# Kernel tuning notes

Hardware: AMD Instinct MI355X
Metric: run time of the kernel (lower is better)

The kernel has to match this reference:

```python
import jax, jax.numpy as jnp
import numpy as np

H = 256  # hidden_dim
NH = 4   # num_heads
HD = H // NH  # head dim


def setup_inputs() -> dict:
    key = jax.random.key(0)
    ks = jax.random.split(key, 12)
    B, TD, ID = 65536, 512, 512
    s_t = 1.0 / np.sqrt(TD)
    s_h = 1.0 / np.sqrt(H)
    s_f = 1.0 / np.sqrt(2 * H)
    return {
        "text_features": jax.random.normal(ks[0], (B, TD), jnp.float32),
        "image_features": jax.random.normal(ks[1], (B, ID), jnp.float32),
        "W_text": jax.random.uniform(ks[2], (H, TD), jnp.float32, -s_t, s_t),
        "b_text": jax.random.uniform(ks[3], (H,), jnp.float32, -s_t, s_t),
        "W_img": jax.random.uniform(ks[4], (H, ID), jnp.float32, -s_t, s_t),
        "b_img": jax.random.uniform(ks[5], (H,), jnp.float32, -s_t, s_t),
        "in_proj_w": jax.random.normal(ks[6], (3 * H, H), jnp.float32) * s_h,  # xavier-ish
        "in_proj_b": jnp.zeros((3 * H,), jnp.float32),
        "out_proj_w": jax.random.uniform(ks[7], (H, H), jnp.float32, -s_h, s_h),
        "out_proj_b": jnp.zeros((H,), jnp.float32),
        "W_fuse": jax.random.uniform(ks[8], (H, 2 * H), jnp.float32, -s_f, s_f),
        "b_fuse": jax.random.uniform(ks[9], (H,), jnp.float32, -s_f, s_f),
    }


def _mha_seq1(q_in, kv_in, in_proj_w, in_proj_b, out_proj_w, out_proj_b):
    """nn.MultiheadAttention with query seq_len=1 and kv seq_len=1 (eval mode).
    q_in, kv_in: [B, H]. Softmax over the single key is identically 1."""
    Wq, Wk, Wv = jnp.split(in_proj_w, 3, axis=0)
    bq, bk, bv = jnp.split(in_proj_b, 3, axis=0)
    q = (q_in @ Wq.T + bq).reshape(-1, NH, HD)   # [B, nh, hd]
    k = (kv_in @ Wk.T + bk).reshape(-1, NH, HD)
    v = (kv_in @ Wv.T + bv).reshape(-1, NH, HD)
    scores = jnp.einsum("bnd,bnd->bn", q, k) / np.sqrt(HD)  # [B, nh], one key
    attn = jax.nn.softmax(scores[..., None], axis=-1)       # == 1 exactly
    out = (attn * v).reshape(-1, H)                          # concat heads
    return out @ out_proj_w.T + out_proj_b


def reference(text_features, image_features, W_text, b_text, W_img, b_img,
              in_proj_w, in_proj_b, out_proj_w, out_proj_b, W_fuse, b_fuse):
    tp = text_features @ W_text.T + b_text      # [B, H]
    ip = image_features @ W_img.T + b_img       # [B, H]
    text_att = _mha_seq1(tp, ip, in_proj_w, in_proj_b, out_proj_w, out_proj_b)
    img_att = _mha_seq1(ip, tp, in_proj_w, in_proj_b, out_proj_w, out_proj_b)
    fused = jnp.concatenate([text_att, img_att], axis=1)  # [B, 2H]
    return jax.nn.relu(fused @ W_fuse.T + b_fuse)          # dropout = eval no-op
```

## Files before the change

kernel.cpp:

```cpp
#include <hip/hip_runtime.h>
#include <hip/hip_bf16.h>

typedef __attribute__((ext_vector_type(4))) float floatx4;
typedef __attribute__((ext_vector_type(8))) __bf16 bf16x8;

__device__ __forceinline__ unsigned short f2bf(float x) {
    union { float f; unsigned u; } v; v.f = x;
    unsigned r = v.u + 0x7fffu + ((v.u >> 16) & 1u);
    return (unsigned short)(r >> 16);
}

__global__ void p1_M_c(const float* __restrict__ out_proj_w,
                       const float* __restrict__ out_proj_b,
                       const float* __restrict__ in_proj_w,
                       const float* __restrict__ in_proj_b,
                       float* __restrict__ Mmat, float* __restrict__ cvec) {
    __shared__ float row[256];
    __shared__ float red[256];
    const int i = blockIdx.x, j = threadIdx.x;
    row[j] = out_proj_w[i * 256 + j];
    __syncthreads();
    const float* Wv = in_proj_w + 512 * 256;
    float acc = 0.f;
    #pragma unroll 8
    for (int k = 0; k < 256; ++k) acc = fmaf(row[k], Wv[k * 256 + j], acc);
    Mmat[i * 256 + j] = acc;
    red[j] = row[j] * in_proj_b[512 + j];
    __syncthreads();
    for (int s = 128; s > 0; s >>= 1) {
        if (j < s) red[j] += red[j + s];
        __syncthreads();
    }
    if (j == 0) cvec[i] = red[0] + out_proj_b[i];
}

__global__ void p2_G(const float* __restrict__ W_fuse, const float* __restrict__ Mmat,
                     float* __restrict__ G) {
    __shared__ float row[256];
    const int b = blockIdx.x, j = threadIdx.x;
    const int half = b >> 8, i = b & 255;
    row[j] = W_fuse[i * 512 + half * 256 + j];
    __syncthreads();
    float acc = 0.f;
    #pragma unroll 8
    for (int k = 0; k < 256; ++k) acc = fmaf(row[k], Mmat[k * 256 + j], acc);
    G[half * 65536 + i * 256 + j] = acc;
}

__global__ void p3_A(const float* __restrict__ G,
                     const float* __restrict__ W_img, const float* __restrict__ W_text,
                     const float* __restrict__ W_fuse,
                     const float* __restrict__ b_img, const float* __restrict__ b_text,
                     const float* __restrict__ b_fuse, const float* __restrict__ cvec,
                     unsigned short* __restrict__ Wt, float* __restrict__ b_total) {
    __shared__ float grow[4][256];
    __shared__ float red[256];
    const int b = blockIdx.x, j = threadIdx.x;
    const int half = b & 1;
    const int n0 = (b >> 1) * 4;
    const float* Gh = G + half * 65536;
    #pragma unroll
    for (int rr = 0; rr < 4; ++rr) grow[rr][j] = Gh[(n0 + rr) * 256 + j];
    __syncthreads();
    const float* Wsrc = half ? W_text : W_img;
    float acc0[4] = {0.f, 0.f, 0.f, 0.f}, acc1[4] = {0.f, 0.f, 0.f, 0.f};
    #pragma unroll 4
    for (int m = 0; m < 256; ++m) {
        float w0 = Wsrc[m * 512 + j];
        float w1 = Wsrc[m * 512 + 256 + j];
        #pragma unroll
        for (int rr = 0; rr < 4; ++rr) {
            float g = grow[rr][m];
            acc0[rr] = fmaf(g, w0, acc0[rr]);
            acc1[rr] = fmaf(g, w1, acc1[rr]);
        }
    }
    #pragma unroll
    for (int rr = 0; rr < 4; ++rr) {
        const int n = n0 + rr;
        const int nt = n >> 4, nl = n & 15;
        {
            const int kg = half * 512 + j;
            const int kq = kg >> 5, q = (kg >> 3) & 3, jj = kg & 7;
            Wt[((nt * 32 + kq) * 64 + q * 16 + nl) * 8 + jj] = f2bf(acc0[rr]);
        }
        {
            const int kg = half * 512 + 256 + j;
            const int kq = kg >> 5, q = (kg >> 3) & 3, jj = kg & 7;
            Wt[((nt * 32 + kq) * 64 + q * 16 + nl) * 8 + jj] = f2bf(acc1[rr]);
        }
    }
    if (half == 0) {
        const float* Gi = G;
        const float* Gt = G + 65536;
        for (int rr = 0; rr < 4; ++rr) {
            const int n = n0 + rr;
            red[j] = Gi[n * 256 + j] * b_img[j] + Gt[n * 256 + j] * b_text[j]
                   + (W_fuse[n * 512 + j] + W_fuse[n * 512 + 256 + j]) * cvec[j];
            __syncthreads();
            for (int s = 128; s > 0; s >>= 1) {
                if (j < s) red[j] += red[j + s];
                __syncthreads();
            }
            if (j == 0) b_total[n] = b_fuse[n] + red[0];
            __syncthreads();
        }
    }
}

__global__ __launch_bounds__(256, 2)
void fused_gemm(const float* __restrict__ Ximg, const float* __restrict__ Xtxt,
                const unsigned short* __restrict__ Wt,
                const float* __restrict__ b_total, float* __restrict__ out) {
    __shared__ unsigned short At[2][128 * 64];
    const int bid = blockIdx.x;
    const int rowtile = bid >> 1;
    const int cb = bid & 1;
    const int rowbase = rowtile * 128;
    const int t = threadIdx.x;
    const int lane = t & 63;
    const int wave = t >> 6;
    const int wr = wave >> 1, wc = wave & 1;
    const int ml = lane & 15, q = lane >> 4;
    const int xr = ml & 7;
    const int sr = t >> 4;
    const int sc4 = t & 15;
    const int ntbase = cb * 8 + wc * 4;

    floatx4 ld[8];
    floatx4 acc[4][4];
    #pragma unroll
    for (int a = 0; a < 4; ++a)
        #pragma unroll
        for (int bq = 0; bq < 4; ++bq) acc[a][bq] = (floatx4){0.f, 0.f, 0.f, 0.f};

    auto load_step = [&](int s) {
        const int kb = (s & 7) * 64;
        const float* X = (s < 8) ? Ximg : Xtxt;
        const float* src = X + (size_t)(rowbase + sr) * 512 + kb + sc4 * 4;
        #pragma unroll
        for (int i = 0; i < 8; ++i)
            ld[i] = *(const floatx4*)(src + (size_t)i * 16 * 512);
    };
    auto store_tile = [&](unsigned short* buf) {
        const int c = sc4 >> 1;
        const int hofs = (sc4 & 1) * 4;
        #pragma unroll
        for (int i = 0; i < 8; ++i) {
            const int r = sr + 16 * i;
            const int chunk = c ^ (r & 7);
            float2 p0; p0.x = ld[i].x; p0.y = ld[i].y;
            float2 p1; p1.x = ld[i].z; p1.y = ld[i].w;
            __hip_bfloat162 v0 = __float22bfloat162_rn(p0);
            __hip_bfloat162 v1 = __float22bfloat162_rn(p1);
            __hip_bfloat162* dst = (__hip_bfloat162*)(buf + r * 64 + chunk * 8 + hofs);
            dst[0] = v0;
            dst[1] = v1;
        }
    };
    auto compute_step = [&](const unsigned short* buf, int s) {
        #pragma unroll
        for (int koi = 0; koi < 2; ++koi) {
            bf16x8 af[4];
            #pragma unroll
            for (int mi = 0; mi < 4; ++mi) {
                const int r = wr * 64 + mi * 16 + ml;
                const int chunk = ((koi << 2) | q) ^ xr;
                af[mi] = *(const bf16x8*)(buf + r * 64 + chunk * 8);
            }
            const int kq = 2 * s + koi;
            bf16x8 bfr[4];
            #pragma unroll
            for (int ni = 0; ni < 4; ++ni)
                bfr[ni] = *(const bf16x8*)(Wt + (size_t)((ntbase + ni) * 32 + kq) * 512 + lane * 8);
            #pragma unroll
            for (int mi = 0; mi < 4; ++mi)
                #pragma unroll
                for (int ni = 0; ni < 4; ++ni)
                    acc[mi][ni] = __builtin_amdgcn_mfma_f32_16x16x32_bf16(af[mi], bfr[ni], acc[mi][ni], 0, 0, 0);
        }
    };

    load_step(0);
    store_tile(At[0]);
    for (int s = 0; s < 16; ++s) {
        __syncthreads();
        if (s < 15) load_step(s + 1);
        compute_step(At[s & 1], s);
        if (s < 15) store_tile(At[(s + 1) & 1]);
    }

    const int colbase = cb * 128 + wc * 64;
    #pragma unroll
    for (int ni = 0; ni < 4; ++ni) {
        const int col = colbase + ni * 16 + ml;
        const float bias = b_total[col];
        #pragma unroll
        for (int mi = 0; mi < 4; ++mi) {
            const size_t r0 = (size_t)rowbase + wr * 64 + mi * 16 + q * 4;
            #pragma unroll
            for (int e = 0; e < 4; ++e) {
                float v = acc[mi][ni][e] + bias;
                out[(r0 + e) * 256 + col] = fmaxf(v, 0.f);
            }
        }
    }
}

extern "C" void kernel_launch(void* const* d_in, const int* in_sizes, int n_in,
                              void* d_out, int out_size, void* d_ws, size_t ws_size,
                              hipStream_t stream) {
    const float* text       = (const float*)d_in[0];
    const float* image      = (const float*)d_in[1];
    const float* W_text     = (const float*)d_in[2];
    const float* b_text     = (const float*)d_in[3];
    const float* W_img      = (const float*)d_in[4];
    const float* b_img      = (const float*)d_in[5];
    const float* in_proj_w  = (const float*)d_in[6];
    const float* in_proj_b  = (const float*)d_in[7];
    const float* out_proj_w = (const float*)d_in[8];
    const float* out_proj_b = (const float*)d_in[9];
    const float* W_fuse     = (const float*)d_in[10];
    const float* b_fuse     = (const float*)d_in[11];
    float* out = (float*)d_out;

    float* ws      = (float*)d_ws;
    float* Mmat    = ws;
    float* G       = ws + 65536;
    float* cvec    = ws + 3 * 65536;
    float* b_total = cvec + 256;
    unsigned short* Wt = (unsigned short*)(b_total + 256);

    p1_M_c<<<dim3(256), dim3(256), 0, stream>>>(out_proj_w, out_proj_b, in_proj_w, in_proj_b, Mmat, cvec);
    p2_G<<<dim3(512), dim3(256), 0, stream>>>(W_fuse, Mmat, G);
    p3_A<<<dim3(128), dim3(256), 0, stream>>>(G, W_img, W_text, W_fuse, b_img, b_text, b_fuse, cvec, Wt, b_total);
    fused_gemm<<<dim3(1024), dim3(256), 0, stream>>>(image, text, Wt, b_total, out);
}
```

Before: 404.6 us.

## Reassociate weight folding into tiled GEMMs and make main GEMM LDS-free

The weight-folding precompute is re-associated and split differently. One kernel forms W_fuse·out_proj and Wv·W_img/W_text as shared-memory-tiled SGEMMs, plus the bias vectors. A second tiled kernel multiplies those products into the packed bf16 weight and the total bias. This replaces three poorly parallel row-per-block kernels with two launches. The main MFMA GEMM drops the LDS staging and swizzle: each wave loads its 32 activation rows straight from global into registers, converts them to bf16, and covers 128 output columns with double-buffered register prefetch. The trade-off is less data sharing between waves, more register pressure and possibly less coalesced global reads.

```diff
diff --git a/kernel.cpp b/kernel.cpp
--- a/kernel.cpp
+++ b/kernel.cpp
@@ -2,7 +2,9 @@
 #include <hip/hip_bf16.h>
 
 typedef __attribute__((ext_vector_type(4))) float floatx4;
+typedef __attribute__((ext_vector_type(2))) float floatx2;
 typedef __attribute__((ext_vector_type(8))) __bf16 bf16x8;
+typedef __attribute__((ext_vector_type(8))) unsigned short ushortx8;
 
 __device__ __forceinline__ unsigned short f2bf(float x) {
     union { float f; unsigned u; } v; v.f = x;
@@ -10,194 +12,219 @@
     return (unsigned short)(r >> 16);
 }
 
-__global__ void p1_M_c(const float* __restrict__ out_proj_w,
-                       const float* __restrict__ out_proj_b,
-                       const float* __restrict__ in_proj_w,
-                       const float* __restrict__ in_proj_b,
-                       float* __restrict__ Mmat, float* __restrict__ cvec) {
-    __shared__ float row[256];
-    __shared__ float red[256];
-    const int i = blockIdx.x, j = threadIdx.x;
-    row[j] = out_proj_w[i * 256 + j];
-    __syncthreads();
-    const float* Wv = in_proj_w + 512 * 256;
-    float acc = 0.f;
-    #pragma unroll 8
-    for (int k = 0; k < 256; ++k) acc = fmaf(row[k], Wv[k * 256 + j], acc);
-    Mmat[i * 256 + j] = acc;
-    red[j] = row[j] * in_proj_b[512 + j];
-    __syncthreads();
-    for (int s = 128; s > 0; s >>= 1) {
-        if (j < s) red[j] += red[j + s];
-        __syncthreads();
-    }
-    if (j == 0) cvec[i] = red[0] + out_proj_b[i];
-}
-
-__global__ void p2_G(const float* __restrict__ W_fuse, const float* __restrict__ Mmat,
-                     float* __restrict__ G) {
-    __shared__ float row[256];
-    const int b = blockIdx.x, j = threadIdx.x;
-    const int half = b >> 8, i = b & 255;
-    row[j] = W_fuse[i * 512 + half * 256 + j];
-    __syncthreads();
-    float acc = 0.f;
-    #pragma unroll 8
-    for (int k = 0; k < 256; ++k) acc = fmaf(row[k], Mmat[k * 256 + j], acc);
-    G[half * 65536 + i * 256 + j] = acc;
-}
-
-__global__ void p3_A(const float* __restrict__ G,
-                     const float* __restrict__ W_img, const float* __restrict__ W_text,
-                     const float* __restrict__ W_fuse,
-                     const float* __restrict__ b_img, const float* __restrict__ b_text,
-                     const float* __restrict__ b_fuse, const float* __restrict__ cvec,
+__device__ __forceinline__ bf16x8 as_bf(ushortx8 v) {
+    union { ushortx8 u; bf16x8 b; } x; x.u = v; return x.b;
+}
+
+__device__ __forceinline__ bf16x8 cvt8(floatx4 lo, floatx4 hi) {
+    union { bf16x8 v; __hip_bfloat162 h[4]; } u;
+    float2 p;
+    p.x = lo.x; p.y = lo.y; u.h[0] = __float22bfloat162_rn(p);
+    p.x = lo.z; p.y = lo.w; u.h[1] = __float22bfloat162_rn(p);
+    p.x = hi.x; p.y = hi.y; u.h[2] = __float22bfloat162_rn(p);
+    p.x = hi.z; p.y = hi.w; u.h[3] = __float22bfloat162_rn(p);
+    return u.v;
+}
+
+__global__ void k1_tree(const float* __restrict__ W_fuse, const float* __restrict__ OP,
+                        const float* __restrict__ ipw, const float* __restrict__ ipb,
+                        const float* __restrict__ W_img, const float* __restrict__ W_text,
+                        const float* __restrict__ opb, const float* __restrict__ b_img,
+                        const float* __restrict__ b_text,
+                        float* __restrict__ U0, float* __restrict__ U1,
+                        float* __restrict__ Vimg, float* __restrict__ Vtxt,
+                        float* __restrict__ vb_img, float* __restrict__ vb_txt,
+                        float* __restrict__ cvec) {
+    const int bid = blockIdx.x;
+    const int t = threadIdx.x;
+    const float* Wv = ipw + 512 * 256;
+    if (bid == 96) {
+        if (t < 256) {
+            float a0 = opb[t], a1 = 0.f, a2 = 0.f;
+            const float* oprow = OP + t * 256;
+            const float* wvrow = Wv + t * 256;
+            #pragma unroll 4
+            for (int k = 0; k < 256; ++k) {
+                a0 = fmaf(oprow[k], ipb[512 + k], a0);
+                a1 = fmaf(wvrow[k], b_img[k], a1);
+                a2 = fmaf(wvrow[k], b_text[k], a2);
+            }
+            cvec[t] = a0; vb_img[t] = a1; vb_txt[t] = a2;
+        }
+        return;
+    }
+    const float *A, *B; float* C; int lda, ldb, ldc, aoff, tm, tn;
+    if (bid < 32) {
+        int h = bid >> 4, tt = bid & 15;
+        A = W_fuse; lda = 512; aoff = h * 256;
+        B = OP; ldb = 256; C = h ? U1 : U0; ldc = 256;
+        tm = tt >> 2; tn = tt & 3;
+    } else {
+        int b2 = bid - 32; int h = b2 >> 5; int tt = b2 & 31;
+        A = Wv; lda = 256; aoff = 0;
+        B = h ? W_text : W_img; ldb = 512; C = h ? Vtxt : Vimg; ldc = 512;
+        tm = tt >> 3; tn = tt & 7;
+    }
+    __shared__ float As[16][68];
+    __shared__ float Bs[16][68];
+    const int arow = t >> 3, ak = (t & 7) * 2;
+    const int brow = t >> 5, bc = (t & 31) * 2;
+    const int ty = t >> 4, tx = t & 15;
+    float acc[2][4] = {};
+    for (int k0 = 0; k0 < 256; k0 += 16) {
+        floatx2 av = *(const floatx2*)(A + (size_t)(tm * 64 + arow) * lda + aoff + k0 + ak);
+        floatx2 bv = *(const floatx2*)(B + (size_t)(k0 + brow) * ldb + tn * 64 + bc);
+        __syncthreads();
+        As[ak + 0][arow] = av.x;
+        As[ak + 1][arow] = av.y;
+        *(floatx2*)&Bs[brow][bc] = bv;
+        __syncthreads();
+        #pragma unroll
+        for (int kk = 0; kk < 16; ++kk) {
+            floatx2 a = *(const floatx2*)&As[kk][ty * 2];
+            floatx4 b = *(const floatx4*)&Bs[kk][tx * 4];
+            acc[0][0] = fmaf(a.x, b.x, acc[0][0]); acc[0][1] = fmaf(a.x, b.y, acc[0][1]);
+            acc[0][2] = fmaf(a.x, b.z, acc[0][2]); acc[0][3] = fmaf(a.x, b.w, acc[0][3]);
+            acc[1][0] = fmaf(a.y, b.x, acc[1][0]); acc[1][1] = fmaf(a.y, b.y, acc[1][1]);
+            acc[1][2] = fmaf(a.y, b.z, acc[1][2]); acc[1][3] = fmaf(a.y, b.w, acc[1][3]);
+        }
+    }
+    #pragma unroll
+    for (int i = 0; i < 2; ++i) {
+        floatx4 o; o.x = acc[i][0]; o.y = acc[i][1]; o.z = acc[i][2]; o.w = acc[i][3];
+        *(floatx4*)(C + (size_t)(tm * 64 + ty * 2 + i) * ldc + tn * 64 + tx * 4) = o;
+    }
+}
+
+__global__ void k2_A(const float* __restrict__ U0, const float* __restrict__ U1,
+                     const float* __restrict__ Vimg, const float* __restrict__ Vtxt,
+                     const float* __restrict__ W_fuse, const float* __restrict__ b_fuse,
+                     const float* __restrict__ vb_img, const float* __restrict__ vb_txt,
+                     const float* __restrict__ cvec,
                      unsigned short* __restrict__ Wt, float* __restrict__ b_total) {
-    __shared__ float grow[4][256];
-    __shared__ float red[256];
-    const int b = blockIdx.x, j = threadIdx.x;
-    const int half = b & 1;
-    const int n0 = (b >> 1) * 4;
-    const float* Gh = G + half * 65536;
-    #pragma unroll
-    for (int rr = 0; rr < 4; ++rr) grow[rr][j] = Gh[(n0 + rr) * 256 + j];
-    __syncthreads();
-    const float* Wsrc = half ? W_text : W_img;
-    float acc0[4] = {0.f, 0.f, 0.f, 0.f}, acc1[4] = {0.f, 0.f, 0.f, 0.f};
-    #pragma unroll 4
-    for (int m = 0; m < 256; ++m) {
-        float w0 = Wsrc[m * 512 + j];
-        float w1 = Wsrc[m * 512 + 256 + j];
-        #pragma unroll
-        for (int rr = 0; rr < 4; ++rr) {
-            float g = grow[rr][m];
-            acc0[rr] = fmaf(g, w0, acc0[rr]);
-            acc1[rr] = fmaf(g, w1, acc1[rr]);
-        }
-    }
-    #pragma unroll
-    for (int rr = 0; rr < 4; ++rr) {
-        const int n = n0 + rr;
-        const int nt = n >> 4, nl = n & 15;
-        {
-            const int kg = half * 512 + j;
-            const int kq = kg >> 5, q = (kg >> 3) & 3, jj = kg & 7;
-            Wt[((nt * 32 + kq) * 64 + q * 16 + nl) * 8 + jj] = f2bf(acc0[rr]);
-        }
-        {
-            const int kg = half * 512 + 256 + j;
-            const int kq = kg >> 5, q = (kg >> 3) & 3, jj = kg & 7;
-            Wt[((nt * 32 + kq) * 64 + q * 16 + nl) * 8 + jj] = f2bf(acc1[rr]);
-        }
-    }
-    if (half == 0) {
-        const float* Gi = G;
-        const float* Gt = G + 65536;
-        for (int rr = 0; rr < 4; ++rr) {
-            const int n = n0 + rr;
-            red[j] = Gi[n * 256 + j] * b_img[j] + Gt[n * 256 + j] * b_text[j]
-                   + (W_fuse[n * 512 + j] + W_fuse[n * 512 + 256 + j]) * cvec[j];
-            __syncthreads();
-            for (int s = 128; s > 0; s >>= 1) {
-                if (j < s) red[j] += red[j + s];
-                __syncthreads();
+    const int bid = blockIdx.x;
+    const int t = threadIdx.x;
+    if (bid == 64) {
+        if (t < 256) {
+            float acc = b_fuse[t];
+            const float* u0 = U0 + t * 256;
+            const float* u1 = U1 + t * 256;
+            const float* wf = W_fuse + t * 512;
+            #pragma unroll 4
+            for (int j = 0; j < 256; ++j) {
+                acc = fmaf(u0[j], vb_img[j], acc);
+                acc = fmaf(u1[j], vb_txt[j], acc);
+                acc = fmaf(wf[j] + wf[j + 256], cvec[j], acc);
             }
-            if (j == 0) b_total[n] = b_fuse[n] + red[0];
-            __syncthreads();
-        }
-    }
+            b_total[t] = acc;
+        }
+        return;
+    }
+    const int h = bid >> 5, tt = bid & 31;
+    const float* A = h ? U1 : U0;
+    const float* B = h ? Vtxt : Vimg;
+    const int tm = tt >> 3, tn = tt & 7;
+    __shared__ float As[16][68];
+    __shared__ float Bs[16][68];
+    const int arow = t >> 3, ak = (t & 7) * 2;
+    const int brow = t >> 5, bc = (t & 31) * 2;
+    const int n_l = t >> 3, oct = t & 7;
+    float acc[8] = {};
+    for (int k0 = 0; k0 < 256; k0 += 16) {
+        floatx2 av = *(const floatx2*)(A + (size_t)(tm * 64 + arow) * 256 + k0 + ak);
+        floatx2 bv = *(const floatx2*)(B + (size_t)(k0 + brow) * 512 + tn * 64 + bc);
+        __syncthreads();
+        As[ak + 0][arow] = av.x;
+        As[ak + 1][arow] = av.y;
+        *(floatx2*)&Bs[brow][bc] = bv;
+        __syncthreads();
+        #pragma unroll
+        for (int kk = 0; kk < 16; ++kk) {
+            float u = As[kk][n_l];
+            floatx4 v0 = *(const floatx4*)&Bs[kk][oct * 8];
+            floatx4 v1 = *(const floatx4*)&Bs[kk][oct * 8 + 4];
+            acc[0] = fmaf(u, v0.x, acc[0]); acc[1] = fmaf(u, v0.y, acc[1]);
+            acc[2] = fmaf(u, v0.z, acc[2]); acc[3] = fmaf(u, v0.w, acc[3]);
+            acc[4] = fmaf(u, v1.x, acc[4]); acc[5] = fmaf(u, v1.y, acc[5]);
+            acc[6] = fmaf(u, v1.z, acc[6]); acc[7] = fmaf(u, v1.w, acc[7]);
+        }
+    }
+    const int n = tm * 64 + n_l;
+    const int kg = h * 512 + tn * 64 + oct * 8;
+    const int kq = kg >> 5, q = (kg >> 3) & 3;
+    const int nt = n >> 4, nl = n & 15;
+    union { ushortx8 v; unsigned short s[8]; } o;
+    #pragma unroll
+    for (int j = 0; j < 8; ++j) o.s[j] = f2bf(acc[j]);
+    *(ushortx8*)&Wt[(size_t)((nt * 32 + kq) * 64 + q * 16 + nl) * 8] = o.v;
 }
 
 __global__ __launch_bounds__(256, 2)
 void fused_gemm(const float* __restrict__ Ximg, const float* __restrict__ Xtxt,
                 const unsigned short* __restrict__ Wt,
                 const float* __restrict__ b_total, float* __restrict__ out) {
-    __shared__ unsigned short At[2][128 * 64];
     const int bid = blockIdx.x;
-    const int rowtile = bid >> 1;
-    const int cb = bid & 1;
-    const int rowbase = rowtile * 128;
-    const int t = threadIdx.x;
-    const int lane = t & 63;
-    const int wave = t >> 6;
-    const int wr = wave >> 1, wc = wave & 1;
+    const int rowtile = bid >> 1, cb = bid & 1;
+    const int t = threadIdx.x, lane = t & 63, w = t >> 6;
     const int ml = lane & 15, q = lane >> 4;
-    const int xr = ml & 7;
-    const int sr = t >> 4;
-    const int sc4 = t & 15;
-    const int ntbase = cb * 8 + wc * 4;
-
-    floatx4 ld[8];
-    floatx4 acc[4][4];
-    #pragma unroll
-    for (int a = 0; a < 4; ++a)
-        #pragma unroll
-        for (int bq = 0; bq < 4; ++bq) acc[a][bq] = (floatx4){0.f, 0.f, 0.f, 0.f};
-
-    auto load_step = [&](int s) {
-        const int kb = (s & 7) * 64;
-        const float* X = (s < 8) ? Ximg : Xtxt;
-        const float* src = X + (size_t)(rowbase + sr) * 512 + kb + sc4 * 4;
-        #pragma unroll
-        for (int i = 0; i < 8; ++i)
-            ld[i] = *(const floatx4*)(src + (size_t)i * 16 * 512);
+    const size_t rowbase = (size_t)rowtile * 128 + w * 32;
+    const size_t roff0 = (rowbase + ml) * 512 + q * 8;
+    const size_t roff1 = roff0 + (size_t)16 * 512;
+    const unsigned short* wbase = Wt + ((size_t)(cb * 8) * 32) * 512 + lane * 8;
+
+    floatx4 acc[2][8];
+    #pragma unroll
+    for (int mi = 0; mi < 2; ++mi)
+        #pragma unroll
+        for (int ni = 0; ni < 8; ++ni) acc[mi][ni] = (floatx4){0.f, 0.f, 0.f, 0.f};
+
+    floatx4 aA[2][2], aB[2][2];
+
+    auto loadA = [&](int idx, floatx4 (&dst)[2][2]) {
+        const float* X = (idx < 16) ? Ximg : Xtxt;
+        const size_t ko = (size_t)(idx & 15) * 32;
+        dst[0][0] = *(const floatx4*)(X + roff0 + ko);
+        dst[0][1] = *(const floatx4*)(X + roff0 + ko + 4);
+        dst[1][0] = *(const floatx4*)(X + roff1 + ko);
+        dst[1][1] = *(const floatx4*)(X + roff1 + ko + 4);
     };
-    auto store_tile = [&](unsigned short* buf) {
-        const int c = sc4 >> 1;
-        const int hofs = (sc4 & 1) * 4;
-        #pragma unroll
-        for (int i = 0; i < 8; ++i) {
-            const int r = sr + 16 * i;
-            const int chunk = c ^ (r & 7);
-            float2 p0; p0.x = ld[i].x; p0.y = ld[i].y;
-            float2 p1; p1.x = ld[i].z; p1.y = ld[i].w;
-            __hip_bfloat162 v0 = __float22bfloat162_rn(p0);
-            __hip_bfloat162 v1 = __float22bfloat162_rn(p1);
-            __hip_bfloat162* dst = (__hip_bfloat162*)(buf + r * 64 + chunk * 8 + hofs);
-            dst[0] = v0;
-            dst[1] = v1;
-        }
+    auto loadB = [&](int kq, ushortx8 (&bf)[8]) {
+        const unsigned short* p = wbase + (size_t)kq * 512;
+        #pragma unroll
+        for (int ni = 0; ni < 8; ++ni) bf[ni] = *(const ushortx8*)(p + (size_t)ni * 32 * 512);
     };
-    auto compute_step = [&](const unsigned short* buf, int s) {
-        #pragma unroll
-        for (int koi = 0; koi < 2; ++koi) {
-            bf16x8 af[4];
+    auto docompute = [&](floatx4 (&af32)[2][2], ushortx8 (&bf)[8]) {
+        bf16x8 af[2];
+        #pragma unroll
+        for (int mi = 0; mi < 2; ++mi) af[mi] = cvt8(af32[mi][0], af32[mi][1]);
+        #pragma unroll
+        for (int mi = 0; mi < 2; ++mi)
             #pragma unroll
-            for (int mi = 0; mi < 4; ++mi) {
-                const int r = wr * 64 + mi * 16 + ml;
-                const int chunk = ((koi << 2) | q) ^ xr;
-                af[mi] = *(const bf16x8*)(buf + r * 64 + chunk * 8);
-            }
-            const int kq = 2 * s + koi;
-            bf16x8 bfr[4];
-            #pragma unroll
-            for (int ni = 0; ni < 4; ++ni)
-                bfr[ni] = *(const bf16x8*)(Wt + (size_t)((ntbase + ni) * 32 + kq) * 512 + lane * 8);
-            #pragma unroll
-            for (int mi = 0; mi < 4; ++mi)
-                #pragma unroll
-                for (int ni = 0; ni < 4; ++ni)
-                    acc[mi][ni] = __builtin_amdgcn_mfma_f32_16x16x32_bf16(af[mi], bfr[ni], acc[mi][ni], 0, 0, 0);
-        }
+            for (int ni = 0; ni < 8; ++ni)
+                acc[mi][ni] = __builtin_amdgcn_mfma_f32_16x16x32_bf16(af[mi], as_bf(bf[ni]), acc[mi][ni], 0, 0, 0);
     };
 
-    load_step(0);
-    store_tile(At[0]);
-    for (int s = 0; s < 16; ++s) {
-        __syncthreads();
-        if (s < 15) load_step(s + 1);
-        compute_step(At[s & 1], s);
-        if (s < 15) store_tile(At[(s + 1) & 1]);
-    }
-
-    const int colbase = cb * 128 + wc * 64;
-    #pragma unroll
-    for (int ni = 0; ni < 4; ++ni) {
+    loadA(0, aA);
+    #pragma unroll 2
+    for (int kq = 0; kq < 32; kq += 2) {
+        ushortx8 b0[8];
+        loadB(kq, b0);
+        loadA(kq + 1, aB);
+        docompute(aA, b0);
+        ushortx8 b1[8];
+        loadB(kq + 1, b1);
+        loadA(kq + 2, aA);
+        docompute(aB, b1);
+    }
+
+    const int colbase = cb * 128;
+    #pragma unroll
+    for (int ni = 0; ni < 8; ++ni) {
         const int col = colbase + ni * 16 + ml;
         const float bias = b_total[col];
         #pragma unroll
-        for (int mi = 0; mi < 4; ++mi) {
-            const size_t r0 = (size_t)rowbase + wr * 64 + mi * 16 + q * 4;
+        for (int mi = 0; mi < 2; ++mi) {
+            const size_t r0 = rowbase + mi * 16 + q * 4;
             #pragma unroll
             for (int e = 0; e < 4; ++e) {
                 float v = acc[mi][ni][e] + bias;
@@ -225,14 +252,20 @@
     float* out = (float*)d_out;
 
     float* ws      = (float*)d_ws;
-    float* Mmat    = ws;
-    float* G       = ws + 65536;
-    float* cvec    = ws + 3 * 65536;
-    float* b_total = cvec + 256;
-    unsigned short* Wt = (unsigned short*)(b_total + 256);
-
-    p1_M_c<<<dim3(256), dim3(256), 0, stream>>>(out_proj_w, out_proj_b, in_proj_w, in_proj_b, Mmat, cvec);
-    p2_G<<<dim3(512), dim3(256), 0, stream>>>(W_fuse, Mmat, G);
-    p3_A<<<dim3(128), dim3(256), 0, stream>>>(G, W_img, W_text, W_fuse, b_img, b_text, b_fuse, cvec, Wt, b_total);
+    float* U0      = ws;
+    float* U1      = ws + 65536;
+    float* Vimg    = ws + 131072;
+    float* Vtxt    = ws + 262144;
+    float* vb_img  = ws + 393216;
+    float* vb_txt  = ws + 393472;
+    float* cvec    = ws + 393728;
+    float* b_total = ws + 393984;
+    unsigned short* Wt = (unsigned short*)(ws + 394240);
+
+    k1_tree<<<dim3(97), dim3(512), 0, stream>>>(W_fuse, out_proj_w, in_proj_w, in_proj_b,
+                                                W_img, W_text, out_proj_b, b_img, b_text,
+                                                U0, U1, Vimg, Vtxt, vb_img, vb_txt, cvec);
+    k2_A<<<dim3(65), dim3(512), 0, stream>>>(U0, U1, Vimg, Vtxt, W_fuse, b_fuse,
+                                             vb_img, vb_txt, cvec, Wt, b_total);
     fused_gemm<<<dim3(1024), dim3(256), 0, stream>>>(image, text, Wt, b_total, out);
 }
```

Result: slower. 441.3 us (+9.1%).
